# Kernel optimization log

Hardware: AMD Instinct MI355X
Metric: run time of the kernel (lower is better)

The kernel has to match this reference:

```python
import jax, jax.numpy as jnp
import numpy as np

B, Q, C, H = 4, 256, 1024, 128
NEG_SLOPE = 0.01  # F.leaky_relu default


def setup_inputs() -> dict:
    key = jax.random.key(0)
    ks = jax.random.split(key, 6)
    return {
        "query": jax.random.normal(ks[0], (B, Q, H), dtype=jnp.float32),
        "context": jax.random.normal(ks[1], (B, C, H), dtype=jnp.float32),
        "Ww": jax.random.normal(ks[2], (H, 2 * H), dtype=jnp.float32) * 0.05,
        "bw": jax.random.normal(ks[3], (H,), dtype=jnp.float32) * 0.05,
        "Ws": jax.random.normal(ks[4], (1, H), dtype=jnp.float32) * 0.05,
        "bs": jax.random.normal(ks[5], (1,), dtype=jnp.float32) * 0.05,
    }


def reference(query, context, Ww, bw, Ws, bs):
    # Faithful to: leaky_relu(Linear(cat(q_expand, c_expand))) then score, softmax, bmm.
    # cat+linear is split into per-input projections (mathematically identical),
    # avoiding the (B,Q,C,2H) concat materialization.
    h = query.shape[-1]
    Wq, Wc = Ww[:, :h], Ww[:, h:]
    hq = jnp.einsum('bqh,kh->bqk', query, Wq)            # (B,Q,H)
    hc = jnp.einsum('bch,kh->bck', context, Wc) + bw     # (B,C,H)
    hidden = jax.nn.leaky_relu(hq[:, :, None, :] + hc[:, None, :, :], NEG_SLOPE)  # (B,Q,C,H)
    score = jnp.einsum('bqch,oh->bqc', hidden, Ws) + bs[0]  # (B,Q,C)
    attn = jax.nn.softmax(score, axis=-1)                   # (B,Q,C)
    attn_output = jnp.einsum('bqc,bch->bqh', attn, context)  # mix=True bmm
    return (attn_output, attn)
```

## Files before the change

kernel.cpp:

```cpp
#include <hip/hip_runtime.h>

#define B_   4
#define Q_   256
#define C_   1024
#define H_   128
#define NEG  0.01f

__global__ __launch_bounds__(128) void proj_kernel(
    const float* __restrict__ query, const float* __restrict__ context,
    const float* __restrict__ Ww, const float* __restrict__ bw,
    float* __restrict__ hq, float* __restrict__ hc)
{
    const int blk = blockIdx.x;
    const int k = threadIdx.x;
    const bool is_q = (blk < (B_ * Q_ / 8));
    const int row0 = is_q ? (blk * 8) : ((blk - B_ * Q_ / 8) * 8);
    const float* __restrict__ in = is_q ? query : context;
    float* __restrict__ out = is_q ? hq : hc;

    const float4* __restrict__ Wrow =
        reinterpret_cast<const float4*>(Ww + k * (2 * H_) + (is_q ? 0 : H_));
    const float4* __restrict__ in4 =
        reinterpret_cast<const float4*>(in + row0 * H_);

    float acc[8] = {0.f, 0.f, 0.f, 0.f, 0.f, 0.f, 0.f, 0.f};
    #pragma unroll 8
    for (int h4 = 0; h4 < H_ / 4; ++h4) {
        const float4 wvv = Wrow[h4];
        #pragma unroll
        for (int r = 0; r < 8; ++r) {
            const float4 iv = in4[r * (H_ / 4) + h4];
            acc[r] += iv.x * wvv.x + iv.y * wvv.y + iv.z * wvv.z + iv.w * wvv.w;
        }
    }
    const float bias = is_q ? 0.f : bw[k];
    #pragma unroll
    for (int r = 0; r < 8; ++r)
        out[(row0 + r) * H_ + k] = acc[r] + bias;
}

__global__ __launch_bounds__(512) void attn_kernel(
    const float* __restrict__ hq, const float* __restrict__ hc,
    const float* __restrict__ Ws, const float* __restrict__ context,
    float* __restrict__ outA, float* __restrict__ outP)
{
    const int b  = blockIdx.x >> 6;
    const int q0 = (blockIdx.x & 63) * 4;
    const int t  = threadIdx.x;
    const int wv = t >> 6;

    __shared__ float4 attn4_s[C_];
    __shared__ float  red[16 * 4 * H_];
    __shared__ float  wred[8][4];
    __shared__ float  wsum[8][4];

    const float4* __restrict__ hq4  = reinterpret_cast<const float4*>(hq);
    const float4* __restrict__ hc4  = reinterpret_cast<const float4*>(hc);
    const float4* __restrict__ ws4  = reinterpret_cast<const float4*>(Ws);
    const float4* __restrict__ ctx4 = reinterpret_cast<const float4*>(context);

    float s[4][2] = {{0.f,0.f},{0.f,0.f},{0.f,0.f},{0.f,0.f}};
    const int c0 = t, c1 = t + 512;
    #pragma unroll 4
    for (int k0 = 0; k0 < H_ / 4; ++k0) {
        const float4 wsv = ws4[k0];
        float4 hqv[4];
        #pragma unroll
        for (int q = 0; q < 4; ++q)
            hqv[q] = hq4[(b * Q_ + q0 + q) * (H_ / 4) + k0];
        #pragma unroll
        for (int ci = 0; ci < 2; ++ci) {
            const int c = ci ? c1 : c0;
            const float4 hcv = hc4[(b * C_ + c) * (H_ / 4) + k0];
            #pragma unroll
            for (int q = 0; q < 4; ++q) {
                float x0 = hqv[q].x + hcv.x;
                float x1 = hqv[q].y + hcv.y;
                float x2 = hqv[q].z + hcv.z;
                float x3 = hqv[q].w + hcv.w;
                x0 = fmaxf(x0, NEG * x0);
                x1 = fmaxf(x1, NEG * x1);
                x2 = fmaxf(x2, NEG * x2);
                x3 = fmaxf(x3, NEG * x3);
                s[q][ci] += wsv.x * x0 + wsv.y * x1 + wsv.z * x2 + wsv.w * x3;
            }
        }
    }

    float m[4];
    #pragma unroll
    for (int q = 0; q < 4; ++q) {
        float v = fmaxf(s[q][0], s[q][1]);
        #pragma unroll
        for (int off = 32; off >= 1; off >>= 1)
            v = fmaxf(v, __shfl_xor(v, off, 64));
        m[q] = v;
    }
    if ((t & 63) == 0) {
        #pragma unroll
        for (int q = 0; q < 4; ++q) wred[wv][q] = m[q];
    }
    __syncthreads();
    #pragma unroll
    for (int q = 0; q < 4; ++q) {
        float v = wred[0][q];
        #pragma unroll
        for (int i = 1; i < 8; ++i) v = fmaxf(v, wred[i][q]);
        m[q] = v;
    }
    float e[4][2], p[4];
    #pragma unroll
    for (int q = 0; q < 4; ++q) {
        e[q][0] = __expf(s[q][0] - m[q]);
        e[q][1] = __expf(s[q][1] - m[q]);
        float v = e[q][0] + e[q][1];
        #pragma unroll
        for (int off = 32; off >= 1; off >>= 1)
            v += __shfl_xor(v, off, 64);
        p[q] = v;
    }
    if ((t & 63) == 0) {
        #pragma unroll
        for (int q = 0; q < 4; ++q) wsum[wv][q] = p[q];
    }
    __syncthreads();
    float rS[4];
    #pragma unroll
    for (int q = 0; q < 4; ++q) {
        float S = wsum[0][q];
        #pragma unroll
        for (int i = 1; i < 8; ++i) S += wsum[i][q];
        rS[q] = 1.0f / S;
    }
    float a0[4], a1[4];
    #pragma unroll
    for (int q = 0; q < 4; ++q) {
        a0[q] = e[q][0] * rS[q];
        a1[q] = e[q][1] * rS[q];
    }
    attn4_s[c0] = make_float4(a0[0], a0[1], a0[2], a0[3]);
    attn4_s[c1] = make_float4(a1[0], a1[1], a1[2], a1[3]);
    #pragma unroll
    for (int q = 0; q < 4; ++q) {
        outP[(b * Q_ + q0 + q) * C_ + c0] = a0[q];
        outP[(b * Q_ + q0 + q) * C_ + c1] = a1[q];
    }
    __syncthreads();

    const int hg   = t & 31;
    const int crep = t >> 5;
    float4 acc[4] = {{0,0,0,0},{0,0,0,0},{0,0,0,0},{0,0,0,0}};
    const int cb = crep * 64;
    #pragma unroll 4
    for (int cc = 0; cc < 64; ++cc) {
        const int c = cb + cc;
        const float4 a4 = attn4_s[c];
        const float4 xv = ctx4[(b * C_ + c) * (H_ / 4) + hg];
        acc[0].x += a4.x * xv.x; acc[0].y += a4.x * xv.y; acc[0].z += a4.x * xv.z; acc[0].w += a4.x * xv.w;
        acc[1].x += a4.y * xv.x; acc[1].y += a4.y * xv.y; acc[1].z += a4.y * xv.z; acc[1].w += a4.y * xv.w;
        acc[2].x += a4.z * xv.x; acc[2].y += a4.z * xv.y; acc[2].z += a4.z * xv.z; acc[2].w += a4.z * xv.w;
        acc[3].x += a4.w * xv.x; acc[3].y += a4.w * xv.y; acc[3].z += a4.w * xv.z; acc[3].w += a4.w * xv.w;
    }
    float4* red4 = reinterpret_cast<float4*>(red);
    #pragma unroll
    for (int q = 0; q < 4; ++q)
        red4[(crep * 4 + q) * 32 + hg] = acc[q];
    __syncthreads();
    {
        const int q = t >> 7, h = t & 127;
        float v = 0.f;
        #pragma unroll
        for (int cr = 0; cr < 16; ++cr)
            v += red[(cr * 4 + q) * H_ + h];
        outA[(b * Q_ + q0 + q) * H_ + h] = v;
    }
}

extern "C" void kernel_launch(void* const* d_in, const int* in_sizes, int n_in,
                              void* d_out, int out_size, void* d_ws, size_t ws_size,
                              hipStream_t stream) {
    const float* query   = (const float*)d_in[0];
    const float* context = (const float*)d_in[1];
    const float* Ww      = (const float*)d_in[2];
    const float* bw      = (const float*)d_in[3];
    const float* Ws      = (const float*)d_in[4];

    float* outA = (float*)d_out;
    float* outP = outA + B_ * Q_ * H_;

    float* hq = (float*)d_ws;
    float* hc = hq + B_ * Q_ * H_;

    hipLaunchKernelGGL(proj_kernel, dim3(640), dim3(128), 0, stream,
                       query, context, Ww, bw, hq, hc);
    hipLaunchKernelGGL(attn_kernel, dim3(256), dim3(512), 0, stream,
                       hq, hc, Ws, context, outA, outP);
}
```

Measured before the change: 109.6 us.

## Store projections transposed (H-major) so score loop reads coalesced float2 per thread

The projection kernel now tiles 64 rows into LDS and writes hq/hc transposed as (B,H,R), so in the attention score loop each thread loads a contiguous float2 of two adjacent context positions per k instead of a strided float4 row. Each thread now owns contexts 2t and 2t+1, which lets the attn writes become float2 stores. The aim is coalesced global loads in the dominant score loop, in exchange for a reworked projection kernel that reads Ww per-thread from global memory.

```diff
diff --git a/kernel.cpp b/kernel.cpp
--- a/kernel.cpp
+++ b/kernel.cpp
@@ -6,41 +6,57 @@
 #define H_   128
 #define NEG  0.01f
 
-__global__ __launch_bounds__(128) void proj_kernel(
+__global__ __launch_bounds__(256) void proj_kernel(
     const float* __restrict__ query, const float* __restrict__ context,
     const float* __restrict__ Ww, const float* __restrict__ bw,
-    float* __restrict__ hq, float* __restrict__ hc)
+    float* __restrict__ hq_t, float* __restrict__ hc_t)
 {
-    const int blk = blockIdx.x;
-    const int k = threadIdx.x;
-    const bool is_q = (blk < (B_ * Q_ / 8));
-    const int row0 = is_q ? (blk * 8) : ((blk - B_ * Q_ / 8) * 8);
-    const float* __restrict__ in = is_q ? query : context;
-    float* __restrict__ out = is_q ? hq : hc;
-
-    const float4* __restrict__ Wrow =
-        reinterpret_cast<const float4*>(Ww + k * (2 * H_) + (is_q ? 0 : H_));
-    const float4* __restrict__ in4 =
-        reinterpret_cast<const float4*>(in + row0 * H_);
-
-    float acc[8] = {0.f, 0.f, 0.f, 0.f, 0.f, 0.f, 0.f, 0.f};
+    const int x = blockIdx.x;
+    const int t = threadIdx.x;
+    const bool is_c = (x < 256);
+    int b, tile, ks, R, w_off;
+    const float* __restrict__ in;
+    float* __restrict__ out;
+    if (is_c) { b = x >> 6; tile = (x >> 2) & 15; ks = x & 3; R = C_; w_off = 32; in = context; out = hc_t; }
+    else { const int y = x - 256; b = y >> 4; tile = (y >> 2) & 3; ks = y & 3; R = Q_; w_off = 0; in = query; out = hq_t; }
+    const int c0 = tile * 64;
+
+    __shared__ float4 lds[64 * 33];
+
+    const float4* __restrict__ in4 = reinterpret_cast<const float4*>(in);
+    const float4* __restrict__ Ww4 = reinterpret_cast<const float4*>(Ww);
+
+    #pragma unroll
+    for (int i = 0; i < 8; ++i) {
+        const int idx = t + i * 256;
+        const int row = idx >> 5, col = idx & 31;
+        lds[row * 33 + col] = in4[(b * R + c0 + row) * 32 + col];
+    }
+    __syncthreads();
+
+    const int c  = t & 63;
+    const int kg = t >> 6;
+    const int kb = ks * 32 + kg * 8;
+
+    float acc[8] = {0.f,0.f,0.f,0.f,0.f,0.f,0.f,0.f};
     #pragma unroll 8
-    for (int h4 = 0; h4 < H_ / 4; ++h4) {
-        const float4 wvv = Wrow[h4];
-        #pragma unroll
-        for (int r = 0; r < 8; ++r) {
-            const float4 iv = in4[r * (H_ / 4) + h4];
-            acc[r] += iv.x * wvv.x + iv.y * wvv.y + iv.z * wvv.z + iv.w * wvv.w;
+    for (int h4 = 0; h4 < 32; ++h4) {
+        const float4 cv = lds[c * 33 + h4];
+        #pragma unroll
+        for (int j = 0; j < 8; ++j) {
+            const float4 w = Ww4[(kb + j) * 64 + w_off + h4];
+            acc[j] += cv.x * w.x + cv.y * w.y + cv.z * w.z + cv.w * w.w;
         }
     }
-    const float bias = is_q ? 0.f : bw[k];
-    #pragma unroll
-    for (int r = 0; r < 8; ++r)
-        out[(row0 + r) * H_ + k] = acc[r] + bias;
+    #pragma unroll
+    for (int j = 0; j < 8; ++j) {
+        const float bias = is_c ? bw[kb + j] : 0.f;
+        out[(b * H_ + kb + j) * R + c0 + c] = acc[j] + bias;
+    }
 }
 
 __global__ __launch_bounds__(512) void attn_kernel(
-    const float* __restrict__ hq, const float* __restrict__ hc,
+    const float* __restrict__ hq_t, const float* __restrict__ hc_t,
     const float* __restrict__ Ws, const float* __restrict__ context,
     float* __restrict__ outA, float* __restrict__ outP)
 {
@@ -54,37 +70,30 @@
     __shared__ float  wred[8][4];
     __shared__ float  wsum[8][4];
 
-    const float4* __restrict__ hq4  = reinterpret_cast<const float4*>(hq);
-    const float4* __restrict__ hc4  = reinterpret_cast<const float4*>(hc);
-    const float4* __restrict__ ws4  = reinterpret_cast<const float4*>(Ws);
+    const float4* __restrict__ hq4  = reinterpret_cast<const float4*>(hq_t);
+    const float2* __restrict__ hc2  = reinterpret_cast<const float2*>(hc_t);
     const float4* __restrict__ ctx4 = reinterpret_cast<const float4*>(context);
 
     float s[4][2] = {{0.f,0.f},{0.f,0.f},{0.f,0.f},{0.f,0.f}};
-    const int c0 = t, c1 = t + 512;
+    const int q04 = q0 >> 2;
     #pragma unroll 4
-    for (int k0 = 0; k0 < H_ / 4; ++k0) {
-        const float4 wsv = ws4[k0];
-        float4 hqv[4];
-        #pragma unroll
-        for (int q = 0; q < 4; ++q)
-            hqv[q] = hq4[(b * Q_ + q0 + q) * (H_ / 4) + k0];
-        #pragma unroll
-        for (int ci = 0; ci < 2; ++ci) {
-            const int c = ci ? c1 : c0;
-            const float4 hcv = hc4[(b * C_ + c) * (H_ / 4) + k0];
-            #pragma unroll
-            for (int q = 0; q < 4; ++q) {
-                float x0 = hqv[q].x + hcv.x;
-                float x1 = hqv[q].y + hcv.y;
-                float x2 = hqv[q].z + hcv.z;
-                float x3 = hqv[q].w + hcv.w;
-                x0 = fmaxf(x0, NEG * x0);
-                x1 = fmaxf(x1, NEG * x1);
-                x2 = fmaxf(x2, NEG * x2);
-                x3 = fmaxf(x3, NEG * x3);
-                s[q][ci] += wsv.x * x0 + wsv.y * x1 + wsv.z * x2 + wsv.w * x3;
-            }
-        }
+    for (int k = 0; k < H_; ++k) {
+        const float  wsk = Ws[k];
+        const float4 hqv = hq4[(b * H_ + k) * (Q_ / 4) + q04];
+        const float2 hv  = hc2[(b * H_ + k) * (C_ / 2) + t];
+        float x, y;
+        x = hqv.x + hv.x; y = hqv.x + hv.y;
+        x = fmaxf(x, NEG * x); y = fmaxf(y, NEG * y);
+        s[0][0] += wsk * x; s[0][1] += wsk * y;
+        x = hqv.y + hv.x; y = hqv.y + hv.y;
+        x = fmaxf(x, NEG * x); y = fmaxf(y, NEG * y);
+        s[1][0] += wsk * x; s[1][1] += wsk * y;
+        x = hqv.z + hv.x; y = hqv.z + hv.y;
+        x = fmaxf(x, NEG * x); y = fmaxf(y, NEG * y);
+        s[2][0] += wsk * x; s[2][1] += wsk * y;
+        x = hqv.w + hv.x; y = hqv.w + hv.y;
+        x = fmaxf(x, NEG * x); y = fmaxf(y, NEG * y);
+        s[3][0] += wsk * x; s[3][1] += wsk * y;
     }
 
     float m[4];
@@ -138,13 +147,12 @@
         a0[q] = e[q][0] * rS[q];
         a1[q] = e[q][1] * rS[q];
     }
-    attn4_s[c0] = make_float4(a0[0], a0[1], a0[2], a0[3]);
-    attn4_s[c1] = make_float4(a1[0], a1[1], a1[2], a1[3]);
-    #pragma unroll
-    for (int q = 0; q < 4; ++q) {
-        outP[(b * Q_ + q0 + q) * C_ + c0] = a0[q];
-        outP[(b * Q_ + q0 + q) * C_ + c1] = a1[q];
-    }
+    attn4_s[2 * t]     = make_float4(a0[0], a0[1], a0[2], a0[3]);
+    attn4_s[2 * t + 1] = make_float4(a1[0], a1[1], a1[2], a1[3]);
+    float2* __restrict__ outP2 = reinterpret_cast<float2*>(outP);
+    #pragma unroll
+    for (int q = 0; q < 4; ++q)
+        outP2[(b * Q_ + q0 + q) * (C_ / 2) + t] = make_float2(a0[q], a1[q]);
     __syncthreads();
 
     const int hg   = t & 31;
@@ -188,11 +196,11 @@
     float* outA = (float*)d_out;
     float* outP = outA + B_ * Q_ * H_;
 
-    float* hq = (float*)d_ws;
-    float* hc = hq + B_ * Q_ * H_;
-
-    hipLaunchKernelGGL(proj_kernel, dim3(640), dim3(128), 0, stream,
-                       query, context, Ww, bw, hq, hc);
+    float* hq_t = (float*)d_ws;
+    float* hc_t = hq_t + B_ * H_ * Q_;
+
+    hipLaunchKernelGGL(proj_kernel, dim3(320), dim3(256), 0, stream,
+                       query, context, Ww, bw, hq_t, hc_t);
     hipLaunchKernelGGL(attn_kernel, dim3(256), dim3(512), 0, stream,
-                       hq, hc, Ws, context, outA, outP);
+                       hq_t, hc_t, Ws, context, outA, outP);
 }
```

Measured after the change: 109.8 us. No clear change (+0.2%).
